# Optimization experiments

Measured on AMD Instinct MI355X. Metric: run time of the kernel, lower is better.

The kernel has to match this reference:

```python
import jax, jax.numpy as jnp
import numpy as np

# Sparse MinkUNet-style backbone sizes
N0, N1, N2, N3 = 100000, 50000, 25000, 12500  # voxels per level (batch-concatenated)
K, KD = 27, 8        # 3x3x3 kernel offsets, stride-2 child offsets
B, S = 8, 1024       # batch, seed_num
C0, C1, C2, C3 = 32, 64, 128, 256
COUT = 512


def _w(k, shape, fan_in):
    return jax.random.normal(k, shape, dtype=jnp.float32) / np.sqrt(fan_in)


def setup_inputs() -> dict:
    key = jax.random.key(0)
    ks = jax.random.split(key, 32)
    inp = {}
    inp["feats"] = jax.random.normal(ks[0], (N0, 3), dtype=jnp.float32)
    # neighbor maps (kernel-offset gather indices, as built by a voxel hash map)
    inp["nbr0"] = jax.random.randint(ks[1], (N0, K), 0, N0, dtype=jnp.int32)
    inp["nbr1"] = jax.random.randint(ks[2], (N1, K), 0, N1, dtype=jnp.int32)
    inp["nbr2"] = jax.random.randint(ks[3], (N2, K), 0, N2, dtype=jnp.int32)
    inp["nbr3"] = jax.random.randint(ks[4], (N3, K), 0, N3, dtype=jnp.int32)
    # stride-2 downsample maps (coarse voxel -> fine children)
    inp["down1"] = jax.random.randint(ks[5], (N1, KD), 0, N0, dtype=jnp.int32)
    inp["down2"] = jax.random.randint(ks[6], (N2, KD), 0, N1, dtype=jnp.int32)
    inp["down3"] = jax.random.randint(ks[7], (N3, KD), 0, N2, dtype=jnp.int32)
    # nearest-parent upsample maps (fine voxel -> coarse parent)
    inp["up2"] = jax.random.randint(ks[8], (N2,), 0, N3, dtype=jnp.int32)
    inp["up1"] = jax.random.randint(ks[9], (N1,), 0, N2, dtype=jnp.int32)
    inp["up0"] = jax.random.randint(ks[10], (N0,), 0, N1, dtype=jnp.int32)
    # nearest-voxel devoxelize index for each FPS seed point
    inp["seed_idx"] = jax.random.randint(ks[11], (B, S), 0, N0, dtype=jnp.int32)
    # conv kernels [K, Cin, Cout] and 1x1 (linear) decoder weights
    inp["W_stem"] = _w(ks[12], (K, 3, C0), K * 3)
    inp["W_b0"] = _w(ks[13], (K, C0, C0), K * C0)
    inp["W_d1"] = _w(ks[14], (KD, C0, C1), KD * C0)
    inp["W_b1"] = _w(ks[15], (K, C1, C1), K * C1)
    inp["W_d2"] = _w(ks[16], (KD, C1, C2), KD * C1)
    inp["W_b2"] = _w(ks[17], (K, C2, C2), K * C2)
    inp["W_d3"] = _w(ks[18], (KD, C2, C3), KD * C2)
    inp["W_b3"] = _w(ks[19], (K, C3, C3), K * C3)
    inp["W_u2"] = _w(ks[20], (C3 + C2, 256), C3 + C2)
    inp["W_u1"] = _w(ks[21], (256 + C1, 128), 256 + C1)
    inp["W_u0"] = _w(ks[22], (128 + C0, 96), 128 + C0)
    inp["W_out"] = _w(ks[23], (96, COUT), 96)
    return inp


def sp_conv(f, nbr, W):
    # gather neighbor features then contract over (kernel offset, in-channel)
    g = f[nbr]                                # [N, K, Cin]
    return jnp.einsum('nkc,kco->no', g, W)    # [N, Cout]


def reference(feats, nbr0, nbr1, nbr2, nbr3, down1, down2, down3,
              up2, up1, up0, seed_idx,
              W_stem, W_b0, W_d1, W_b1, W_d2, W_b2, W_d3, W_b3,
              W_u2, W_u1, W_u0, W_out):
    relu = jax.nn.relu
    # encoder
    x0 = relu(sp_conv(feats, nbr0, W_stem))          # [N0, 32]
    x0 = x0 + relu(sp_conv(x0, nbr0, W_b0))
    x1 = relu(sp_conv(x0, down1, W_d1))              # [N1, 64]
    x1 = x1 + relu(sp_conv(x1, nbr1, W_b1))
    x2 = relu(sp_conv(x1, down2, W_d2))              # [N2, 128]
    x2 = x2 + relu(sp_conv(x2, nbr2, W_b2))
    x3 = relu(sp_conv(x2, down3, W_d3))              # [N3, 256]
    x3 = x3 + relu(sp_conv(x3, nbr3, W_b3))
    # decoder: nearest-parent upsample + skip concat + 1x1 conv
    u2 = relu(jnp.concatenate([x3[up2], x2], axis=-1) @ W_u2)   # [N2, 256]
    u1 = relu(jnp.concatenate([u2[up1], x1], axis=-1) @ W_u1)   # [N1, 128]
    u0 = relu(jnp.concatenate([u1[up0], x0], axis=-1) @ W_u0)   # [N0, 96]
    out_vox = u0 @ W_out                                        # [N0, 512]
    seed_feats = out_vox[seed_idx]                              # [B, S, 512]
    return jnp.transpose(seed_feats, (0, 2, 1))                 # [B, 512, S]
```

## Files before the change

kernel.cpp:

```cpp
#include <hip/hip_runtime.h>

typedef unsigned short u16;
typedef unsigned int u32;
typedef __bf16 bf16x8 __attribute__((ext_vector_type(8)));
typedef float f32x4 __attribute__((ext_vector_type(4)));
typedef u16 u16x4 __attribute__((ext_vector_type(4)));

#define NV0 100000
#define NV1 50000
#define NV2 25000
#define NV3 12500

enum : long {
  OFF_WB0  = 0,
  OFF_WD1  = 27648,
  OFF_WB1  = 44032,
  OFF_WD2  = 154624,
  OFF_WB2  = 220160,
  OFF_WD3  = 662528,
  OFF_WB3  = 924672,
  OFF_WU2  = 2694144,
  OFF_WU1  = 2792448,
  OFF_WU0  = 2833408,
  OFF_WOUT = 2848768,
  OFF_TA   = 2897920,
  OFF_X0   = OFF_TA  + 3200000,
  OFF_X1   = OFF_X0  + 3200000,
  OFF_X2   = OFF_X1  + 3200000,
  OFF_X3   = OFF_X2  + 3200000,
  OFF_U2   = OFF_X3  + 3200000,
  OFF_U1   = OFF_U2  + 6400000,
  OFF_U0S  = OFF_U1  + 6400000,
  OFF_END  = OFF_U0S + 786432,
};

__device__ __forceinline__ float b2f(u16 u) {
  union { u32 i; float f; } x; x.i = ((u32)u) << 16; return x.f;
}
__device__ __forceinline__ u16 f2b(float f) {
  union { float f; u32 i; } x; x.f = f;
  u32 r = (x.i + 0x7FFFu + ((x.i >> 16) & 1u)) >> 16;
  return (u16)r;
}
__device__ __forceinline__ void gload16(const u16* g, const u16* l) {
  __builtin_amdgcn_global_load_lds(
      (const __attribute__((address_space(1))) void*)g,
      (__attribute__((address_space(3))) void*)(u16*)l, 16, 0, 0);
}
__device__ __forceinline__ void store_out(u16* p, float v)  { *p = f2b(v); }
__device__ __forceinline__ void store_out(float* p, float v) { *p = v; }
constexpr int ilog2c(int x) { return x <= 1 ? 0 : 1 + ilog2c(x / 2); }

struct PD { const float* src; u16* dst; int KK, CIN, COUT; };
struct PrepArgs { PD d[11]; };

__global__ __launch_bounds__(256) void prep_k(PrepArgs pa) {
  const PD d = pa.d[blockIdx.y];
  const int cc = d.CIN * d.COUT;
  const int total = d.KK * cc;
  for (int e = blockIdx.x * 256 + threadIdx.x; e < total; e += gridDim.x * 256) {
    int k = e / cc;
    int r = e - k * cc;
    int c = r / d.COUT;
    int o = r - c * d.COUT;
    d.dst[(k * d.COUT + o) * d.CIN + c] = f2b(d.src[e]);
  }
}

__global__ __launch_bounds__(256) void stem_k(const float* __restrict__ feats,
                                              const int* __restrict__ nbr0,
                                              const float* __restrict__ wstem,
                                              u16* __restrict__ out) {
  __shared__ float Wl[27 * 3 * 32];
  const int tid = threadIdx.x;
  for (int i = tid; i < 2592; i += 256) Wl[i] = wstem[i];
  __syncthreads();
  const int n = blockIdx.x * 8 + (tid >> 5);
  const int o = tid & 31;
  if (n >= NV0) return;
  float acc = 0.f;
  const int* nb = nbr0 + n * 27;
  #pragma unroll
  for (int k = 0; k < 27; k++) {
    const int iv = nb[k];
    const float* f = feats + iv * 3;
    acc = fmaf(f[0], Wl[(k * 3 + 0) * 32 + o], acc);
    acc = fmaf(f[1], Wl[(k * 3 + 1) * 32 + o], acc);
    acc = fmaf(f[2], Wl[(k * 3 + 2) * 32 + o], acc);
  }
  out[n * 32 + o] = f2b(fmaxf(acc, 0.f));
}

template <int BM, int BN, int WM, int WN, int COUTF, int KCT, int BK, int MODE,
          int CIN, int KK, int CA, int KSPL, bool RES, bool DORELU, typename OT>
__global__ __launch_bounds__(256, 4) void gemm_k(
    const u16* __restrict__ src0, const u16* __restrict__ src1,
    const int* __restrict__ idx0, const int* __restrict__ idx1,
    const u16* __restrict__ wt, const u16* __restrict__ base,
    OT* __restrict__ out, int N) {
  constexpr int NWM = BM / WM, NWN = BN / WN;
  static_assert(NWM * NWN == 4, "4 waves");
  constexpr int MI = WM / 16, NI = WN / 16;
  constexpr int CB = KCT - CA;
  constexpr int SLOTS = BK / 8;
  constexpr int SM = SLOTS - 1;
  constexpr int LSL = ilog2c(SLOTS);
  constexpr int RPC = 64 / SLOTS;
  constexpr int LRPC = ilog2c(RPC);
  constexpr int ACH = (BM * BK) / 512;
  constexpr int BCH = (BN * BK) / 512;
  constexpr int NIT = KCT / BK / KSPL;
  constexpr int LOGC = ilog2c(CIN);
  constexpr int ATRIPS = ACH / 4;
  constexpr int CTRIPS = (ACH + BCH + 3) / 4;
  constexpr int NIDX = (MODE == 0) ? BM * KK : (MODE == 3 ? 1 : 2 * BM);
  static_assert(ACH % 4 == 0, "A chunks divisible by wave count");
  static_assert(KCT % (BK * KSPL) == 0, "K mult of BK*KSPL");
  static_assert((MODE != 1 && MODE != 2) || (CA % BK == 0), "concat boundary aligned");
  static_assert(KSPL == 1 || MODE == 0, "split only for sparse conv");

  __shared__ u16 As[2][BM * BK];
  __shared__ u16 Bs[2][BN * BK];
  __shared__ int Is[NIDX];
  const int tid = threadIdx.x;
  const int w = tid >> 6, lane = tid & 63;
  const int quad = lane >> 4, l16 = lane & 15;
  const int wm = w % NWM, wn = w / NWM;
  const int row0 = blockIdx.x * BM;
  const int col0 = blockIdx.y * BN;
  const int Nm1 = N - 1;
  const int srow = lane >> LSL;
  const int g    = (lane & SM) ^ (srow & SM);
  const int cl   = g * 8;

  if constexpr (MODE == 0) {
    for (int e = tid; e < BM * KK; e += 256) {
      const int r = e / KK, k = e - r * KK;
      int n = row0 + r; n = (n > Nm1) ? Nm1 : n;
      Is[e] = idx0[(long)n * KK + k] * CIN;
    }
  } else if constexpr (MODE == 1) {
    for (int e = tid; e < BM; e += 256) {
      int n = row0 + e; n = (n > Nm1) ? Nm1 : n;
      Is[e] = idx0[n] * CA;
      Is[BM + e] = n * CB;
    }
  } else if constexpr (MODE == 2) {
    for (int e = tid; e < BM; e += 256) {
      int n = row0 + e; n = (n > Nm1) ? Nm1 : n;
      const int s = idx0[n];
      Is[e] = idx1[s] * CA;
      Is[BM + e] = s * CB;
    }
  }
  if constexpr (MODE != 3) __syncthreads();

  int pre[CTRIPS];
  #pragma unroll
  for (int t = 0; t < CTRIPS; t++) {
    const int c = w + 4 * t;
    if (t < ATRIPS) {
      const int r = (c << LRPC) + srow;
      if constexpr (MODE == 0) {
        pre[t] = (r * KK + (cl >> LOGC)) * 4;
      } else if constexpr (MODE == 3) {
        int n = row0 + r; n = (n > Nm1) ? Nm1 : n;
        pre[t] = n * KCT + cl;
      } else {
        pre[t] = r * 4;
      }
    } else if (c < ACH + BCH) {
      const int o = col0 + ((c - ACH) << LRPC) + srow;
      if constexpr (MODE == 0)
        pre[t] = (cl >> LOGC) * (COUTF * CIN) + o * CIN + (cl & (CIN - 1));
      else
        pre[t] = o * KCT + cl;
    }
  }
  const int claneA = (MODE == 0) ? (cl & (CIN - 1)) : cl;

  f32x4 acc[MI][NI];
  #pragma unroll
  for (int i = 0; i < MI; i++)
    #pragma unroll
    for (int j = 0; j < NI; j++) acc[i][j] = {0.f, 0.f, 0.f, 0.f};

  auto stage = [&](int buf, int kc0) {
    int kadd = 0, cadd = 0, kcc = 0;
    const u16* sA = src0;
    if constexpr (MODE == 0) {
      kadd = (kc0 >> LOGC) * 4;
      cadd = kc0 & (CIN - 1);
      kcc  = (kc0 >> LOGC) * (COUTF * CIN) + cadd;
    } else if constexpr (MODE == 1 || MODE == 2) {
      if (kc0 >= CA) { kadd = BM * 4; cadd = kc0 - CA; sA = src1; }
      else           { cadd = kc0; }
    }
    #pragma unroll
    for (int t = 0; t < CTRIPS; t++) {
      const int c = w + 4 * t;
      if constexpr (CTRIPS * 4 > ACH + BCH) { if (c >= ACH + BCH) continue; }
      if (t < ATRIPS) {
        int off;
        if constexpr (MODE == 3) off = pre[t] + kc0;
        else off = *(const int*)((const char*)Is + (pre[t] + kadd)) + cadd + claneA;
        gload16(sA + off, &As[buf][c * 512]);
      } else {
        int off;
        if constexpr (MODE == 0) off = pre[t] + kcc;
        else                     off = pre[t] + kc0;
        gload16(wt + off, &Bs[buf][(c - ACH) * 512]);
      }
    }
  };

  const int kb = (KSPL > 1) ? (int)blockIdx.z * (KCT / KSPL) : 0;
  stage(0, kb);
  #pragma unroll 1
  for (int it = 0; it < NIT; it++) {
    __syncthreads();
    if (it + 1 < NIT) stage((it + 1) & 1, kb + (it + 1) * BK);
    const int buf = it & 1;
    #pragma unroll
    for (int kk = 0; kk < BK / 32; kk++) {
      bf16x8 af[MI], bfr[NI];
      #pragma unroll
      for (int i = 0; i < MI; i++) {
        const int row = wm * WM + i * 16 + l16;
        const int slot = row * SLOTS + (((kk << 2) + quad) ^ (row & SM));
        af[i] = *(const bf16x8*)&As[buf][slot * 8];
      }
      #pragma unroll
      for (int j = 0; j < NI; j++) {
        const int row = wn * WN + j * 16 + l16;
        const int slot = row * SLOTS + (((kk << 2) + quad) ^ (row & SM));
        bfr[j] = *(const bf16x8*)&Bs[buf][slot * 8];
      }
      #pragma unroll
      for (int i = 0; i < MI; i++)
        #pragma unroll
        for (int j = 0; j < NI; j++)
          acc[i][j] = __builtin_amdgcn_mfma_f32_16x16x32_bf16(af[i], bfr[j], acc[i][j], 0, 0, 0);
    }
  }

  OT* op = out;
  if constexpr (KSPL > 1) op += (long)blockIdx.z * ((long)N * COUTF);
  #pragma unroll
  for (int i = 0; i < MI; i++) {
    #pragma unroll
    for (int j = 0; j < NI; j++) {
      const int col = col0 + wn * WN + j * 16 + l16;
      #pragma unroll
      for (int r = 0; r < 4; r++) {
        const int n = row0 + wm * WM + i * 16 + quad * 4 + r;
        if (n < N) {
          float v = acc[i][j][r];
          if constexpr (RES)         v = b2f(base[(long)n * COUTF + col]) + fmaxf(v, 0.f);
          else if constexpr (DORELU) v = fmaxf(v, 0.f);
          store_out(&op[(long)n * COUTF + col], v);
        }
      }
    }
  }
}

__global__ __launch_bounds__(256) void fix_k(const float* __restrict__ p0,
                                             const float* __restrict__ p1,
                                             const u16* __restrict__ base,
                                             u16* __restrict__ out) {
  const long i = ((long)blockIdx.x * 256 + threadIdx.x) * 4;
  const f32x4 a = *(const f32x4*)(p0 + i);
  const f32x4 b = *(const f32x4*)(p1 + i);
  const u16x4 bs = *(const u16x4*)(base + i);
  u16x4 r;
  #pragma unroll
  for (int j = 0; j < 4; j++) r[j] = f2b(b2f(bs[j]) + fmaxf(a[j] + b[j], 0.f));
  *(u16x4*)(out + i) = r;
}

__global__ __launch_bounds__(256) void tout_k(const float* __restrict__ tmp,
                                              float* __restrict__ outp) {
  __shared__ float tl[64][65];
  const int tid = threadIdx.x;
  const int r0 = blockIdx.x * 64, o0 = blockIdx.y * 64;
  {
    const int rl = tid >> 2, oc = (tid & 3) * 16;
    const float* src = &tmp[(r0 + rl) * 512 + o0 + oc];
    #pragma unroll
    for (int j = 0; j < 16; j++) tl[rl][oc + j] = src[j];
  }
  __syncthreads();
  {
    const int ol = tid >> 2, sc = (tid & 3) * 16;
    const int b = r0 >> 10, s0 = r0 & 1023;
    float* dst = &outp[((long)b * 512 + (o0 + ol)) * 1024 + s0 + sc];
    #pragma unroll
    for (int j = 0; j < 16; j++) dst[j] = tl[sc + j][ol];
  }
}

extern "C" void kernel_launch(void* const* d_in, const int* in_sizes, int n_in,
                              void* d_out, int out_size, void* d_ws, size_t ws_size,
                              hipStream_t stream) {
  const float* feats = (const float*)d_in[0];
  const int* nbr0  = (const int*)d_in[1];
  const int* nbr1  = (const int*)d_in[2];
  const int* nbr2  = (const int*)d_in[3];
  const int* nbr3  = (const int*)d_in[4];
  const int* down1 = (const int*)d_in[5];
  const int* down2 = (const int*)d_in[6];
  const int* down3 = (const int*)d_in[7];
  const int* up2   = (const int*)d_in[8];
  const int* up1   = (const int*)d_in[9];
  const int* up0   = (const int*)d_in[10];
  const int* seed  = (const int*)d_in[11];
  u16* ws = (u16*)d_ws;

  PrepArgs pa;
  pa.d[0]  = {(const float*)d_in[13], ws + OFF_WB0,  27, 32, 32};
  pa.d[1]  = {(const float*)d_in[14], ws + OFF_WD1,  8,  32, 64};
  pa.d[2]  = {(const float*)d_in[15], ws + OFF_WB1,  27, 64, 64};
  pa.d[3]  = {(const float*)d_in[16], ws + OFF_WD2,  8,  64, 128};
  pa.d[4]  = {(const float*)d_in[17], ws + OFF_WB2,  27, 128, 128};
  pa.d[5]  = {(const float*)d_in[18], ws + OFF_WD3,  8,  128, 256};
  pa.d[6]  = {(const float*)d_in[19], ws + OFF_WB3,  27, 256, 256};
  pa.d[7]  = {(const float*)d_in[20], ws + OFF_WU2,  1,  384, 256};
  pa.d[8]  = {(const float*)d_in[21], ws + OFF_WU1,  1,  320, 128};
  pa.d[9]  = {(const float*)d_in[22], ws + OFF_WU0,  1,  160, 96};
  pa.d[10] = {(const float*)d_in[23], ws + OFF_WOUT, 1,  96,  512};
  prep_k<<<dim3(128, 11), 256, 0, stream>>>(pa);

  u16* ta  = ws + OFF_TA;
  u16* x0  = ws + OFF_X0;
  u16* x1  = ws + OFF_X1;
  u16* x2  = ws + OFF_X2;
  u16* x3  = ws + OFF_X3;
  u16* u2b = ws + OFF_U2;
  u16* u1b = ws + OFF_U1;
  u16* u0s = ws + OFF_U0S;
  float* tmp  = (float*)(ws + OFF_TA);
  float* part = (float*)(ws + OFF_U2);

  stem_k<<<12500, 256, 0, stream>>>(feats, nbr0, (const float*)d_in[12], ta);

  gemm_k<128, 32, 32, 32, 32, 864, 32, 0, 32, 27, 0, 1, true, true, u16>
      <<<dim3(782, 1), 256, 0, stream>>>(ta, nullptr, nbr0, nullptr, ws + OFF_WB0, ta, x0, NV0);
  gemm_k<64, 64, 32, 32, 64, 256, 64, 0, 32, 8, 0, 1, false, true, u16>
      <<<dim3(782, 1), 256, 0, stream>>>(x0, nullptr, down1, nullptr, ws + OFF_WD1, nullptr, ta, NV1);
  gemm_k<64, 64, 32, 32, 64, 1728, 64, 0, 64, 27, 0, 1, true, true, u16>
      <<<dim3(782, 1), 256, 0, stream>>>(ta, nullptr, nbr1, nullptr, ws + OFF_WB1, ta, x1, NV1);
  gemm_k<64, 64, 32, 32, 128, 512, 64, 0, 64, 8, 0, 1, false, true, u16>
      <<<dim3(391, 2), 256, 0, stream>>>(x1, nullptr, down2, nullptr, ws + OFF_WD2, nullptr, ta, NV2);
  gemm_k<64, 64, 32, 32, 128, 3456, 64, 0, 128, 27, 0, 2, false, false, float>
      <<<dim3(391, 2, 2), 256, 0, stream>>>(ta, nullptr, nbr2, nullptr, ws + OFF_WB2, nullptr, part, NV2);
  fix_k<<<dim3(3125), 256, 0, stream>>>(part, part + 3200000, ta, x2);
  gemm_k<64, 64, 32, 32, 256, 1024, 64, 0, 128, 8, 0, 1, false, true, u16>
      <<<dim3(196, 4), 256, 0, stream>>>(x2, nullptr, down3, nullptr, ws + OFF_WD3, nullptr, ta, NV3);
  gemm_k<64, 64, 32, 32, 256, 6912, 64, 0, 256, 27, 0, 2, false, false, float>
      <<<dim3(196, 4, 2), 256, 0, stream>>>(ta, nullptr, nbr3, nullptr, ws + OFF_WB3, nullptr, part, NV3);
  fix_k<<<dim3(3125), 256, 0, stream>>>(part, part + 3200000, ta, x3);
  gemm_k<64, 64, 32, 32, 256, 384, 64, 1, 32, 1, 256, 1, false, true, u16>
      <<<dim3(391, 4), 256, 0, stream>>>(x3, x2, up2, nullptr, ws + OFF_WU2, nullptr, u2b, NV2);
  gemm_k<64, 64, 32, 32, 128, 320, 64, 1, 32, 1, 256, 1, false, true, u16>
      <<<dim3(782, 2), 256, 0, stream>>>(u2b, x1, up1, nullptr, ws + OFF_WU1, nullptr, u1b, NV1);
  gemm_k<64, 96, 32, 48, 96, 160, 32, 2, 32, 1, 128, 1, false, true, u16>
      <<<dim3(128, 1), 256, 0, stream>>>(u1b, x0, seed, up0, ws + OFF_WU0, nullptr, u0s, 8192);
  gemm_k<64, 64, 32, 32, 512, 96, 32, 3, 32, 1, 0, 1, false, false, float>
      <<<dim3(128, 8), 256, 0, stream>>>(u0s, nullptr, nullptr, nullptr, ws + OFF_WOUT, nullptr, tmp, 8192);
  tout_k<<<dim3(128, 8), 256, 0, stream>>>(tmp, (float*)d_out);
}
```

Measured before the change: 495.6 us.

## Triple-buffer GEMM staging with vmcnt waits and wider tiles for deep convs

New measurement: 603.8 us. +21.8%, slower.

```diff
diff --git a/kernel.cpp b/kernel.cpp
--- a/kernel.cpp
+++ b/kernel.cpp
@@ -51,6 +51,18 @@
 __device__ __forceinline__ void store_out(float* p, float v) { *p = v; }
 constexpr int ilog2c(int x) { return x <= 1 ? 0 : 1 + ilog2c(x / 2); }
 
+template <int N>
+__device__ __forceinline__ void wait_vm() {
+  if constexpr (N <= 0)      asm volatile("s_waitcnt vmcnt(0)" ::: "memory");
+  else if constexpr (N == 1) asm volatile("s_waitcnt vmcnt(1)" ::: "memory");
+  else if constexpr (N == 2) asm volatile("s_waitcnt vmcnt(2)" ::: "memory");
+  else if constexpr (N == 3) asm volatile("s_waitcnt vmcnt(3)" ::: "memory");
+  else if constexpr (N == 4) asm volatile("s_waitcnt vmcnt(4)" ::: "memory");
+  else if constexpr (N == 5) asm volatile("s_waitcnt vmcnt(5)" ::: "memory");
+  else if constexpr (N == 6) asm volatile("s_waitcnt vmcnt(6)" ::: "memory");
+  else                       asm volatile("s_waitcnt vmcnt(7)" ::: "memory");
+}
+
 struct PD { const float* src; u16* dst; int KK, CIN, COUT; };
 struct PrepArgs { PD d[11]; };
 
@@ -100,6 +112,7 @@
     OT* __restrict__ out, int N) {
   constexpr int NWM = BM / WM, NWN = BN / WN;
   static_assert(NWM * NWN == 4, "4 waves");
+  static_assert(BK == 32, "pipeline assumes BK=32");
   constexpr int MI = WM / 16, NI = WN / 16;
   constexpr int CB = KCT - CA;
   constexpr int SLOTS = BK / 8;
@@ -113,14 +126,18 @@
   constexpr int LOGC = ilog2c(CIN);
   constexpr int ATRIPS = ACH / 4;
   constexpr int CTRIPS = (ACH + BCH + 3) / 4;
+  constexpr int TOT = ACH + BCH;
+  constexpr int REM = TOT & 3;
+  constexpr int CLO = TOT >> 2;
   constexpr int NIDX = (MODE == 0) ? BM * KK : (MODE == 3 ? 1 : 2 * BM);
   static_assert(ACH % 4 == 0, "A chunks divisible by wave count");
   static_assert(KCT % (BK * KSPL) == 0, "K mult of BK*KSPL");
   static_assert((MODE != 1 && MODE != 2) || (CA % BK == 0), "concat boundary aligned");
   static_assert(KSPL == 1 || MODE == 0, "split only for sparse conv");
-
-  __shared__ u16 As[2][BM * BK];
-  __shared__ u16 Bs[2][BN * BK];
+  static_assert(NIT >= 2, "pipeline needs >=2 iters");
+
+  __shared__ u16 As[3][BM * BK];
+  __shared__ u16 Bs[3][BN * BK];
   __shared__ int Is[NIDX];
   const int tid = threadIdx.x;
   const int w = tid >> 6, lane = tid & 63;
@@ -130,7 +147,7 @@
   const int col0 = blockIdx.y * BN;
   const int Nm1 = N - 1;
   const int srow = lane >> LSL;
-  const int g    = (lane & SM) ^ (srow & SM);
+  const int g    = (lane & SM) ^ ((srow >> 1) & SM);
   const int cl   = g * 8;
 
   if constexpr (MODE == 0) {
@@ -169,7 +186,7 @@
       } else {
         pre[t] = r * 4;
       }
-    } else if (c < ACH + BCH) {
+    } else if (c < TOT) {
       const int o = col0 + ((c - ACH) << LRPC) + srow;
       if constexpr (MODE == 0)
         pre[t] = (cl >> LOGC) * (COUTF * CIN) + o * CIN + (cl & (CIN - 1));
@@ -199,7 +216,7 @@
     #pragma unroll
     for (int t = 0; t < CTRIPS; t++) {
       const int c = w + 4 * t;
-      if constexpr (CTRIPS * 4 > ACH + BCH) { if (c >= ACH + BCH) continue; }
+      if constexpr (CTRIPS * 4 > TOT) { if (c >= TOT) continue; }
       if (t < ATRIPS) {
         int off;
         if constexpr (MODE == 3) off = pre[t] + kc0;
@@ -216,32 +233,42 @@
 
   const int kb = (KSPL > 1) ? (int)blockIdx.z * (KCT / KSPL) : 0;
   stage(0, kb);
+  stage(1, kb + BK);
+  int bc = 0, bsg = 2;
   #pragma unroll 1
   for (int it = 0; it < NIT; it++) {
-    __syncthreads();
-    if (it + 1 < NIT) stage((it + 1) & 1, kb + (it + 1) * BK);
-    const int buf = it & 1;
-    #pragma unroll
-    for (int kk = 0; kk < BK / 32; kk++) {
+    if (it + 1 < NIT) {
+      if constexpr (REM != 0) {
+        if (w < REM) wait_vm<CLO + 1>(); else wait_vm<CLO>();
+      } else wait_vm<CLO>();
+    } else wait_vm<0>();
+    __builtin_amdgcn_s_barrier();
+    asm volatile("" ::: "memory");
+    if (it + 2 < NIT) stage(bsg, kb + (it + 2) * BK);
+    {
       bf16x8 af[MI], bfr[NI];
       #pragma unroll
       for (int i = 0; i < MI; i++) {
         const int row = wm * WM + i * 16 + l16;
-        const int slot = row * SLOTS + (((kk << 2) + quad) ^ (row & SM));
-        af[i] = *(const bf16x8*)&As[buf][slot * 8];
+        const int slot = row * SLOTS + (quad ^ ((row >> 1) & SM));
+        af[i] = *(const bf16x8*)&As[bc][slot * 8];
       }
       #pragma unroll
       for (int j = 0; j < NI; j++) {
         const int row = wn * WN + j * 16 + l16;
-        const int slot = row * SLOTS + (((kk << 2) + quad) ^ (row & SM));
-        bfr[j] = *(const bf16x8*)&Bs[buf][slot * 8];
-      }
+        const int slot = row * SLOTS + (quad ^ ((row >> 1) & SM));
+        bfr[j] = *(const bf16x8*)&Bs[bc][slot * 8];
+      }
+      __builtin_amdgcn_s_setprio(1);
       #pragma unroll
       for (int i = 0; i < MI; i++)
         #pragma unroll
         for (int j = 0; j < NI; j++)
           acc[i][j] = __builtin_amdgcn_mfma_f32_16x16x32_bf16(af[i], bfr[j], acc[i][j], 0, 0, 0);
-    }
+      __builtin_amdgcn_s_setprio(0);
+    }
+    bc = (bc == 2) ? 0 : bc + 1;
+    bsg = (bsg == 2) ? 0 : bsg + 1;
   }
 
   OT* op = out;
@@ -346,23 +373,23 @@
 
   gemm_k<128, 32, 32, 32, 32, 864, 32, 0, 32, 27, 0, 1, true, true, u16>
       <<<dim3(782, 1), 256, 0, stream>>>(ta, nullptr, nbr0, nullptr, ws + OFF_WB0, ta, x0, NV0);
-  gemm_k<64, 64, 32, 32, 64, 256, 64, 0, 32, 8, 0, 1, false, true, u16>
+  gemm_k<64, 64, 32, 32, 64, 256, 32, 0, 32, 8, 0, 1, false, true, u16>
       <<<dim3(782, 1), 256, 0, stream>>>(x0, nullptr, down1, nullptr, ws + OFF_WD1, nullptr, ta, NV1);
-  gemm_k<64, 64, 32, 32, 64, 1728, 64, 0, 64, 27, 0, 1, true, true, u16>
+  gemm_k<64, 64, 32, 32, 64, 1728, 32, 0, 64, 27, 0, 1, true, true, u16>
       <<<dim3(782, 1), 256, 0, stream>>>(ta, nullptr, nbr1, nullptr, ws + OFF_WB1, ta, x1, NV1);
-  gemm_k<64, 64, 32, 32, 128, 512, 64, 0, 64, 8, 0, 1, false, true, u16>
+  gemm_k<64, 64, 32, 32, 128, 512, 32, 0, 64, 8, 0, 1, false, true, u16>
       <<<dim3(391, 2), 256, 0, stream>>>(x1, nullptr, down2, nullptr, ws + OFF_WD2, nullptr, ta, NV2);
-  gemm_k<64, 64, 32, 32, 128, 3456, 64, 0, 128, 27, 0, 2, false, false, float>
-      <<<dim3(391, 2, 2), 256, 0, stream>>>(ta, nullptr, nbr2, nullptr, ws + OFF_WB2, nullptr, part, NV2);
+  gemm_k<64, 128, 32, 64, 128, 3456, 32, 0, 128, 27, 0, 2, false, false, float>
+      <<<dim3(391, 1, 2), 256, 0, stream>>>(ta, nullptr, nbr2, nullptr, ws + OFF_WB2, nullptr, part, NV2);
   fix_k<<<dim3(3125), 256, 0, stream>>>(part, part + 3200000, ta, x2);
-  gemm_k<64, 64, 32, 32, 256, 1024, 64, 0, 128, 8, 0, 1, false, true, u16>
+  gemm_k<64, 64, 32, 32, 256, 1024, 32, 0, 128, 8, 0, 1, false, true, u16>
       <<<dim3(196, 4), 256, 0, stream>>>(x2, nullptr, down3, nullptr, ws + OFF_WD3, nullptr, ta, NV3);
-  gemm_k<64, 64, 32, 32, 256, 6912, 64, 0, 256, 27, 0, 2, false, false, float>
-      <<<dim3(196, 4, 2), 256, 0, stream>>>(ta, nullptr, nbr3, nullptr, ws + OFF_WB3, nullptr, part, NV3);
+  gemm_k<64, 128, 32, 64, 256, 6912, 32, 0, 256, 27, 0, 2, false, false, float>
+      <<<dim3(196, 2, 2), 256, 0, stream>>>(ta, nullptr, nbr3, nullptr, ws + OFF_WB3, nullptr, part, NV3);
   fix_k<<<dim3(3125), 256, 0, stream>>>(part, part + 3200000, ta, x3);
-  gemm_k<64, 64, 32, 32, 256, 384, 64, 1, 32, 1, 256, 1, false, true, u16>
+  gemm_k<64, 64, 32, 32, 256, 384, 32, 1, 32, 1, 256, 1, false, true, u16>
       <<<dim3(391, 4), 256, 0, stream>>>(x3, x2, up2, nullptr, ws + OFF_WU2, nullptr, u2b, NV2);
-  gemm_k<64, 64, 32, 32, 128, 320, 64, 1, 32, 1, 256, 1, false, true, u16>
+  gemm_k<64, 64, 32, 32, 128, 320, 32, 1, 32, 1, 256, 1, false, true, u16>
       <<<dim3(782, 2), 256, 0, stream>>>(u2b, x1, up1, nullptr, ws + OFF_WU1, nullptr, u1b, NV1);
   gemm_k<64, 96, 32, 48, 96, 160, 32, 2, 32, 1, 128, 1, false, true, u16>
       <<<dim3(128, 1), 256, 0, stream>>>(u1b, x0, seed, up0, ws + OFF_WU0, nullptr, u0s, 8192);
```
